# Optimization experiments

Hardware: AMD Instinct MI355X
Metric: run time of the kernel (lower is better)

Reference implementation:

```python
import jax, jax.numpy as jnp
import numpy as np

B, T, C = 2, 4096, 768
H = 12
HD = C // H  # 64


def setup_inputs() -> dict:
    key = jax.random.key(0)
    k1, k2, k3 = jax.random.split(key, 3)
    scale = 0.02
    x = jax.random.normal(k1, (B, T, C), dtype=jnp.float32)
    w_attn = jax.random.normal(k2, (C, 3 * C), dtype=jnp.float32) * scale
    b_attn = jnp.zeros((3 * C,), dtype=jnp.float32)
    w_proj = jax.random.normal(k3, (C, C), dtype=jnp.float32) * scale
    b_proj = jnp.zeros((C,), dtype=jnp.float32)
    return {"x": x, "w_attn": w_attn, "b_attn": b_attn,
            "w_proj": w_proj, "b_proj": b_proj}


def reference(x, w_attn, b_attn, w_proj, b_proj):
    b, t, c = x.shape
    # QKV projection: (B,T,3C)
    qkv = x @ w_attn + b_attn
    q, k, v = jnp.split(qkv, 3, axis=2)
    # (B,H,T,HD)
    q = q.reshape(b, t, H, HD).transpose(0, 2, 1, 3)
    k = k.reshape(b, t, H, HD).transpose(0, 2, 1, 3)
    v = v.reshape(b, t, H, HD).transpose(0, 2, 1, 3)
    # scores: (B,H,T,T)
    scores = jnp.einsum('bhqd,bhkd->bhqk', q, k) / jnp.sqrt(jnp.float32(HD))
    causal = jnp.tril(jnp.ones((t, t), dtype=bool))
    scores = jnp.where(causal[None, None, :, :], scores, -jnp.inf)
    att = jax.nn.softmax(scores, axis=-1)
    # attn_dropout p=0 -> identity
    y = jnp.einsum('bhqk,bhkd->bhqd', att, v)
    y = y.transpose(0, 2, 1, 3).reshape(b, t, c)
    # output projection (resid_dropout p=0 -> identity)
    return y @ w_proj + b_proj
```

## Files before the change

kernel.cpp:

```cpp
#include <hip/hip_runtime.h>


typedef unsigned short u16;
typedef unsigned int u32;
using bf16x8 = __attribute__((ext_vector_type(8))) short;
using f32x4  = __attribute__((ext_vector_type(4))) float;

__device__ __forceinline__ float bf2f(u16 u) {
  return __uint_as_float(((u32)u) << 16);
}
__device__ __forceinline__ u16 f2bf(float f) {
  u32 u = __float_as_uint(f);
  u += 0x7fffu + ((u >> 16) & 1u);
  return (u16)(u >> 16);
}
__device__ __forceinline__ u32 cvtpk(float lo, float hi) {
  u32 r;
  asm("v_cvt_pk_bf16_f32 %0, %1, %2" : "=v"(r) : "v"(lo), "v"(hi));
  return r;
}
__device__ __forceinline__ void gload_lds16(const u16* g, u16* l) {
  __builtin_amdgcn_global_load_lds(
      (const __attribute__((address_space(1))) unsigned int*)g,
      (__attribute__((address_space(3))) unsigned int*)l, 16, 0, 0);
}

__global__ void fill_sentinel_f32(float* __restrict__ out, int n, float v) {
  const int i0 = blockIdx.x * blockDim.x + threadIdx.x;
  const int stride = gridDim.x * blockDim.x;
  for (int i = i0; i < n; i += stride) out[i] = v;
}

__global__ __launch_bounds__(256)
void prep(const float* __restrict__ x, const float* __restrict__ w_attn,
          const float* __restrict__ b_attn, const float* __restrict__ w_proj,
          const float* __restrict__ b_proj, u16* __restrict__ xb,
          u16* __restrict__ WtA, u16* __restrict__ WtP,
          u16* __restrict__ ba, u16* __restrict__ bp) {
  __shared__ u16 tile[32][33];
  const int bid = blockIdx.x, tid = threadIdx.x;
  if (bid < 2304) {
    const float* in; u16* out; int R, C, bx, by;
    if (bid < 1728) { in = w_attn; out = WtA; R = 768; C = 2304;
                      bx = bid % 72; by = bid / 72; }
    else            { in = w_proj; out = WtP; R = 768; C = 768;
                      bx = (bid - 1728) % 24; by = (bid - 1728) / 24; }
    const int c0 = bx * 32, r0 = by * 32;
    const int tx = tid & 31, ty = tid >> 5;
#pragma unroll
    for (int i = 0; i < 32; i += 8)
      tile[ty + i][tx] = f2bf(in[(size_t)(r0 + ty + i) * C + c0 + tx]);
    __syncthreads();
#pragma unroll
    for (int i = 0; i < 32; i += 8)
      out[(size_t)(c0 + ty + i) * R + r0 + tx] = tile[tx][ty + i];
  } else if (bid < 3328) {
    const int n4 = 8192 * 768 / 4;
    const int i0 = (bid - 2304) * 256 + tid, stride = 1024 * 256;
    const float4* src = (const float4*)x;
    ushort4* dst = (ushort4*)xb;
    for (int i = i0; i < n4; i += stride) {
      const float4 v = src[i];
      ushort4 o;
      o.x = f2bf(v.x); o.y = f2bf(v.y); o.z = f2bf(v.z); o.w = f2bf(v.w);
      dst[i] = o;
    }
  } else {
    for (int i = tid; i < 2304; i += 256) ba[i] = f2bf(b_attn[i]);
    for (int i = tid; i < 768; i += 256) bp[i] = f2bf(b_proj[i]);
  }
}

#define QSCALE 0.18033688011112f

__global__ __launch_bounds__(256, 3)
void gemm128(const u16* __restrict__ A, const u16* __restrict__ Bt,
             const u16* __restrict__ bias, u16* __restrict__ O0,
             u16* __restrict__ O1, u16* __restrict__ O2, int Kd) {
  __shared__ __align__(16) u16 As[128 * 64];
  __shared__ __align__(16) u16 Bs[128 * 64];
  const int tid = threadIdx.x;
  const int lane = tid & 63, wave = tid >> 6;
  const int wm = wave >> 1, wn = wave & 1;
  const int l16 = lane & 15, quad = lane >> 4;

  const u16* Ag0 = A + (size_t)blockIdx.x * 128 * Kd +
                   (size_t)(tid >> 3) * Kd + (tid & 7) * 8;
  const u16* Bg0 = Bt + (size_t)blockIdx.y * 128 * Kd +
                   (size_t)(tid >> 3) * Kd + (tid & 7) * 8;
  const int ldsb = wave * 512;

  f32x4 acc[4][4] = {};
  for (int kt = 0; kt < Kd; kt += 64) {
#pragma unroll
    for (int i = 0; i < 4; ++i) {
      gload_lds16(Ag0 + (size_t)i * 32 * Kd + kt, &As[i * 2048 + ldsb]);
      gload_lds16(Bg0 + (size_t)i * 32 * Kd + kt, &Bs[i * 2048 + ldsb]);
    }
    __syncthreads();
#pragma unroll
    for (int s = 0; s < 2; ++s) {
      bf16x8 af[4], bfr[4];
#pragma unroll
      for (int i = 0; i < 4; ++i) {
        const int m = wm * 64 + i * 16 + l16;
        af[i] = *(const bf16x8*)&As[m * 64 + (s * 4 + quad) * 8];
        const int n = wn * 64 + i * 16 + l16;
        bfr[i] = *(const bf16x8*)&Bs[n * 64 + (s * 4 + quad) * 8];
      }
#pragma unroll
      for (int i = 0; i < 4; ++i)
#pragma unroll
        for (int j = 0; j < 4; ++j)
          acc[i][j] = __builtin_amdgcn_mfma_f32_16x16x32_bf16(af[i], bfr[j],
                                                              acc[i][j], 0, 0, 0);
    }
    __syncthreads();
  }

#pragma unroll
  for (int i = 0; i < 4; ++i) {
    const int mbase = blockIdx.x * 128 + wm * 64 + i * 16 + quad * 4;
#pragma unroll
    for (int j = 0; j < 4; ++j) {
      const int nb = blockIdx.y * 128 + wn * 64 + j * 16;
      const int n = nb + l16;
      const float bv = bf2f(bias[n]);
      const int which = nb / 768;
      const int b = mbase >> 12, t = mbase & 4095;
      const int c = n - which * 768;
      const int h = c >> 6, d = c & 63;
      const size_t bh = (size_t)b * 12 + h;
      if (which == 0) {
#pragma unroll
        for (int r = 0; r < 4; ++r)
          O0[((bh * 4096 + t + r) << 6) + d] =
              f2bf((acc[i][j][r] + bv) * QSCALE);
      } else if (which == 1) {
#pragma unroll
        for (int r = 0; r < 4; ++r)
          O1[((bh * 4096 + t + r) << 6) + d] = f2bf(acc[i][j][r] + bv);
      } else {
        ushort4 pk;
        pk.x = f2bf(acc[i][j][0] + bv);
        pk.y = f2bf(acc[i][j][1] + bv);
        pk.z = f2bf(acc[i][j][2] + bv);
        pk.w = f2bf(acc[i][j][3] + bv);
        *(ushort4*)&O2[((bh << 6) + (size_t)d) * 4096 + t] = pk;
      }
    }
  }
}

__global__ __launch_bounds__(256, 3)
void gemm_n64(const u16* __restrict__ A, const u16* __restrict__ Bt,
              const u16* __restrict__ bias, float* __restrict__ out, int Kd) {
  __shared__ __align__(16) u16 As[128 * 64];
  __shared__ __align__(16) u16 Bs[64 * 64];
  const int tid = threadIdx.x;
  const int lane = tid & 63, wave = tid >> 6;
  const int l16 = lane & 15, quad = lane >> 4;

  const u16* Ag0 = A + (size_t)blockIdx.x * 128 * Kd +
                   (size_t)(tid >> 3) * Kd + (tid & 7) * 8;
  const u16* Bg0 = Bt + (size_t)blockIdx.y * 64 * Kd +
                   (size_t)(tid >> 3) * Kd + (tid & 7) * 8;
  const int ldsb = wave * 512;

  f32x4 acc[2][4] = {};
  for (int kt = 0; kt < Kd; kt += 64) {
#pragma unroll
    for (int i = 0; i < 4; ++i)
      gload_lds16(Ag0 + (size_t)i * 32 * Kd + kt, &As[i * 2048 + ldsb]);
#pragma unroll
    for (int i = 0; i < 2; ++i)
      gload_lds16(Bg0 + (size_t)i * 32 * Kd + kt, &Bs[i * 2048 + ldsb]);
    __syncthreads();
#pragma unroll
    for (int s = 0; s < 2; ++s) {
      bf16x8 af[2], bfr[4];
#pragma unroll
      for (int i = 0; i < 2; ++i) {
        const int m = wave * 32 + i * 16 + l16;
        af[i] = *(const bf16x8*)&As[m * 64 + (s * 4 + quad) * 8];
      }
#pragma unroll
      for (int j = 0; j < 4; ++j) {
        const int n = j * 16 + l16;
        bfr[j] = *(const bf16x8*)&Bs[n * 64 + (s * 4 + quad) * 8];
      }
#pragma unroll
      for (int i = 0; i < 2; ++i)
#pragma unroll
        for (int j = 0; j < 4; ++j)
          acc[i][j] = __builtin_amdgcn_mfma_f32_16x16x32_bf16(af[i], bfr[j],
                                                              acc[i][j], 0, 0, 0);
    }
    __syncthreads();
  }

#pragma unroll
  for (int i = 0; i < 2; ++i) {
    const int mbase = blockIdx.x * 128 + wave * 32 + i * 16 + quad * 4;
#pragma unroll
    for (int j = 0; j < 4; ++j) {
      const int n = blockIdx.y * 64 + j * 16 + l16;
      const float bv = bf2f(bias[n]);
#pragma unroll
      for (int r = 0; r < 4; ++r)
        out[(size_t)(mbase + r) * 768 + n] = acc[i][j][r] + bv;
    }
  }
}

__global__ __launch_bounds__(256, 3)
void attn_chunk(const u16* __restrict__ Q, const u16* __restrict__ K,
                const u16* __restrict__ Vt, u16* __restrict__ Y,
                u16* __restrict__ part_o, float* __restrict__ part_l) {
  const int idx = blockIdx.x;
  const int bh = idx % 24;
  const int cid = 79 - (idx / 24);
  int qt = 0, base = 0, nc = 1;
  for (int q = 0; q < 32; ++q) {
    const int c = (q >> 3) + 1;
    if (cid < base + c) { qt = q; nc = c; break; }
    base += c;
  }
  const int j = cid - base;
  const int Nt = 2 * qt + 2;
  const int kbeg = j * 16;
  const int kend = (kbeg + 16 < Nt) ? kbeg + 16 : Nt;
  const int q0 = qt * 128;
  const int b = bh / 12, h = bh % 12;
  const size_t ho = (size_t)bh * 4096 * 64;
  const u16* Qg = Q + ho + (size_t)q0 * 64;
  const u16* Kg = K + ho;
  const u16* Vg = Vt + ho;

  __shared__ __align__(16) u16 Ks[3][64 * 64];
  __shared__ __align__(16) u16 Vs[3][64 * 64];

  const int tid = threadIdx.x;
  const int lane = tid & 63, wave = tid >> 6;
  const int l16 = lane & 15, quad = lane >> 4;
  const int sw8 = (l16 & 7) * 8;

  const int rl = tid >> 3, m7 = tid & 7;
  const int cs = (m7 ^ (rl & 7)) * 8;
  const u16* kg0 = Kg + (size_t)rl * 64 + cs;
  const u16* vg0 = Vg + (size_t)rl * 4096 + cs;
  const int wb = wave * 512;

  bf16x8 qf[2][2];
#pragma unroll
  for (int rt = 0; rt < 2; ++rt)
#pragma unroll
    for (int s = 0; s < 2; ++s)
      qf[rt][s] = *(const bf16x8*)&Qg[(wave * 32 + rt * 16 + l16) * 64 + s * 32 + quad * 8];

  bf16x8 ones;
#pragma unroll
  for (int e = 0; e < 8; ++e) ones[e] = (short)0x3F80;

  f32x4 lacc[2] = {};
  f32x4 o[2][4] = {};

  auto stage = [&](int bf, int kt2) {
    const size_t ko = (size_t)kt2 * 4096;
    const int to = kt2 * 64;
    gload_lds16(kg0 + ko,               &Ks[bf][wb]);
    gload_lds16(kg0 + ko + 2048,        &Ks[bf][2048 + wb]);
    gload_lds16(vg0 + to,               &Vs[bf][wb]);
    gload_lds16(vg0 + to + 32 * 4096,   &Vs[bf][2048 + wb]);
  };

  const int ntt = kend - kbeg;
  stage(0, kbeg);
  if (ntt > 1) {
    stage(1, kbeg + 1);
    asm volatile("s_waitcnt vmcnt(4)" ::: "memory");
  } else {
    asm volatile("s_waitcnt vmcnt(0)" ::: "memory");
  }
  __builtin_amdgcn_sched_barrier(0);
  __builtin_amdgcn_s_barrier();
  int cur = 0;

  for (int kt2 = kbeg; kt2 < kend; ++kt2) {
    const int t0 = kt2 * 64;
    const bool pf = (kt2 + 2 < kend);
    if (pf) {
      int nb = cur + 2; if (nb >= 3) nb -= 3;
      stage(nb, kt2 + 2);
    }
    __builtin_amdgcn_sched_barrier(0);

    f32x4 sc[4][2] = {};
#pragma unroll
    for (int s = 0; s < 2; ++s) {
      bf16x8 kf[4];
#pragma unroll
      for (int nt = 0; nt < 4; ++nt)
        kf[nt] = *(const bf16x8*)&Ks[cur][(nt * 16 + l16) * 64 +
                                          ((s * 32 + quad * 8) ^ sw8)];
      __builtin_amdgcn_s_setprio(1);
#pragma unroll
      for (int nt = 0; nt < 4; ++nt)
#pragma unroll
        for (int rt = 0; rt < 2; ++rt)
          sc[nt][rt] = __builtin_amdgcn_mfma_f32_16x16x32_bf16(kf[nt], qf[rt][s],
                                                               sc[nt][rt], 0, 0, 0);
      __builtin_amdgcn_s_setprio(0);
    }

    u32 pw[4][2][2];
#pragma unroll
    for (int rt = 0; rt < 2; ++rt) {
      const int rowb = q0 + wave * 32 + rt * 16;
      if (t0 + 63 <= rowb) {
#pragma unroll
        for (int nt = 0; nt < 4; ++nt) {
          f32x4 p;
#pragma unroll
          for (int r = 0; r < 4; ++r)
            p[r] = __builtin_amdgcn_exp2f(sc[nt][rt][r]);
          pw[nt][rt][0] = cvtpk(p[0], p[1]);
          pw[nt][rt][1] = cvtpk(p[2], p[3]);
        }
      } else {
        const int qrow = rowb + l16;
#pragma unroll
        for (int nt = 0; nt < 4; ++nt) {
          f32x4 p;
#pragma unroll
          for (int r = 0; r < 4; ++r) {
            float pv = __builtin_amdgcn_exp2f(sc[nt][rt][r]);
            if (t0 + nt * 16 + quad * 4 + r > qrow) pv = 0.f;
            p[r] = pv;
          }
          pw[nt][rt][0] = cvtpk(p[0], p[1]);
          pw[nt][rt][1] = cvtpk(p[2], p[3]);
        }
      }
    }

#pragma unroll
    for (int s2 = 0; s2 < 2; ++s2) {
      bf16x8 vf[4];
#pragma unroll
      for (int dt = 0; dt < 4; ++dt) {
        const int vbase = (dt * 16 + l16) * 64;
        const int a1 = vbase + ((s2 * 32 + quad * 4) ^ sw8);
        union { uint2 hv[2]; bf16x8 v; } uv;
        uv.hv[0] = *(const uint2*)&Vs[cur][a1];
        uv.hv[1] = *(const uint2*)&Vs[cur][a1 ^ 16];
        vf[dt] = uv.v;
      }
#pragma unroll
      for (int rt = 0; rt < 2; ++rt) {
        union { u32 w[4]; bf16x8 v; } up;
        up.w[0] = pw[2 * s2][rt][0];
        up.w[1] = pw[2 * s2][rt][1];
        up.w[2] = pw[2 * s2 + 1][rt][0];
        up.w[3] = pw[2 * s2 + 1][rt][1];
        __builtin_amdgcn_s_setprio(1);
#pragma unroll
        for (int dt = 0; dt < 4; ++dt)
          o[rt][dt] = __builtin_amdgcn_mfma_f32_16x16x32_bf16(up.v, vf[dt],
                                                              o[rt][dt], 0, 0, 0);
        lacc[rt] = __builtin_amdgcn_mfma_f32_16x16x32_bf16(up.v, ones,
                                                           lacc[rt], 0, 0, 0);
        __builtin_amdgcn_s_setprio(0);
      }
    }

    if (kt2 + 1 < kend) {
      if (pf) asm volatile("s_waitcnt vmcnt(4)" ::: "memory");
      else    asm volatile("s_waitcnt vmcnt(0)" ::: "memory");
      __builtin_amdgcn_sched_barrier(0);
      __builtin_amdgcn_s_barrier();
      if (++cur == 3) cur = 0;
    }
  }

  if (nc == 1) {
#pragma unroll
    for (int rt = 0; rt < 2; ++rt)
#pragma unroll
      for (int r = 0; r < 4; ++r) {
        const float inv = 1.f / lacc[rt][r];
        const int t = q0 + wave * 32 + rt * 16 + quad * 4 + r;
#pragma unroll
        for (int dt = 0; dt < 4; ++dt)
          Y[((size_t)b * 4096 + t) * 768 + h * 64 + dt * 16 + l16] =
              f2bf(o[rt][dt][r] * inv);
      }
  } else {
    const int pslot = bh * 72 + (cid - 8);
    u16* po = part_o + (size_t)pslot * 8192;
    float* pl = part_l + pslot * 128;
#pragma unroll
    for (int rt = 0; rt < 2; ++rt)
#pragma unroll
      for (int r = 0; r < 4; ++r) {
        const int row = wave * 32 + rt * 16 + quad * 4 + r;
#pragma unroll
        for (int dt = 0; dt < 4; ++dt)
          po[row * 64 + dt * 16 + l16] = f2bf(o[rt][dt][r]);
        if (l16 == 0) pl[row] = lacc[rt][r];
      }
  }
}

__global__ __launch_bounds__(256, 8)
void attn_combine(const u16* __restrict__ part_o, const float* __restrict__ part_l,
                  u16* __restrict__ Y) {
  const int bh = blockIdx.x, qt = 8 + blockIdx.y;
  const int g = qt >> 3, i = qt & 7;
  const int nc = g + 1;
  const int base = 4 * g * (g + 1) + i * (g + 1);
  const int slot0 = bh * 72 + base - 8;
  const int b = bh / 12, h = bh % 12;
  const int q0 = qt * 128;
  for (int e = threadIdx.x; e < 8192; e += 256) {
    const int row = e >> 6, d = e & 63;
    float Os = 0.f, ls = 0.f;
    for (int c = 0; c < nc; ++c) {
      Os += bf2f(part_o[(size_t)(slot0 + c) * 8192 + e]);
      ls += part_l[(slot0 + c) * 128 + row];
    }
    Y[((size_t)b * 4096 + q0 + row) * 768 + h * 64 + d] = f2bf(Os / ls);
  }
}

extern "C" void kernel_launch(void* const* d_in, const int* in_sizes, int n_in,
                              void* d_out, int out_size, void* d_ws, size_t ws_size,
                              hipStream_t stream) {
  (void)in_sizes; (void)n_in;
  const float* x      = (const float*)d_in[0];
  const float* w_attn = (const float*)d_in[1];
  const float* b_attn = (const float*)d_in[2];
  const float* w_proj = (const float*)d_in[3];
  const float* b_proj = (const float*)d_in[4];
  float* out = (float*)d_out;

  char* ws = (char*)d_ws;
  size_t off = 0;
  auto alloc = [&](size_t bytes) -> void* {
    void* p = ws + off;
    off += (bytes + 255) & ~(size_t)255;
    return p;
  };
  u16* xb  = (u16*)alloc((size_t)8192 * 768 * 2);
  u16* WtA = (u16*)alloc((size_t)2304 * 768 * 2);
  u16* WtP = (u16*)alloc((size_t)768 * 768 * 2);
  u16* ba  = (u16*)alloc(2304 * 2);
  u16* bp  = (u16*)alloc(768 * 2);
  u16* Q   = (u16*)alloc((size_t)6291456 * 2);
  u16* Kp  = (u16*)alloc((size_t)6291456 * 2);
  u16* Vt  = (u16*)alloc((size_t)6291456 * 2);
  u16* Y   = (u16*)alloc((size_t)6291456 * 2);
  u16* part_o  = (u16*)alloc((size_t)24 * 72 * 8192 * 2);
  float* part_l = (float*)alloc((size_t)24 * 72 * 128 * 4);

  if (ws_size < off) {
    fill_sentinel_f32<<<256, 256, 0, stream>>>(out, out_size,
                                               100.0f + (float)(ws_size >> 20));
    return;
  }

  prep<<<3329, 256, 0, stream>>>(x, w_attn, b_attn, w_proj, b_proj,
                                 xb, WtA, WtP, ba, bp);
  gemm128<<<dim3(64, 18), 256, 0, stream>>>(xb, WtA, ba, Q, Kp, Vt, 768);
  attn_chunk<<<1920, 256, 0, stream>>>(Q, Kp, Vt, Y, part_o, part_l);
  attn_combine<<<dim3(24, 24), 256, 0, stream>>>(part_o, part_l, Y);
  gemm_n64<<<dim3(64, 12), 256, 0, stream>>>(Y, WtP, bp, out, 768);
}
```

Measured before the change: 266.9 us.

## Double-buffer GEMM LDS tiles and XOR-swizzle columns to avoid bank conflicts

Both projection GEMMs now use two LDS buffers and issue the global-to-LDS loads for the next K tile before computing on the current one, with one barrier per iteration instead of two. Source columns are XOR-swizzled by row when loading, and the fragment reads apply the matching swizzle to reduce LDS bank conflicts. gemm128 doubles its LDS use and drops its launch bound from 3 to 2 blocks per CU, which may lower occupancy. Only the GEMMs change; the attention kernel, which likely dominates runtime, is untouched.

```diff
diff --git a/kernel.cpp b/kernel.cpp
--- a/kernel.cpp
+++ b/kernel.cpp
@@ -73,40 +73,52 @@
 
 #define QSCALE 0.18033688011112f
 
-__global__ __launch_bounds__(256, 3)
+__global__ __launch_bounds__(256, 2)
 void gemm128(const u16* __restrict__ A, const u16* __restrict__ Bt,
              const u16* __restrict__ bias, u16* __restrict__ O0,
              u16* __restrict__ O1, u16* __restrict__ O2, int Kd) {
-  __shared__ __align__(16) u16 As[128 * 64];
-  __shared__ __align__(16) u16 Bs[128 * 64];
+  __shared__ __align__(16) u16 As[2][128 * 64];
+  __shared__ __align__(16) u16 Bs[2][128 * 64];
   const int tid = threadIdx.x;
   const int lane = tid & 63, wave = tid >> 6;
   const int wm = wave >> 1, wn = wave & 1;
   const int l16 = lane & 15, quad = lane >> 4;
-
-  const u16* Ag0 = A + (size_t)blockIdx.x * 128 * Kd +
-                   (size_t)(tid >> 3) * Kd + (tid & 7) * 8;
-  const u16* Bg0 = Bt + (size_t)blockIdx.y * 128 * Kd +
-                   (size_t)(tid >> 3) * Kd + (tid & 7) * 8;
+  const int swr = (l16 & 7) * 8;
+
+  const int rl = tid >> 3, m7 = tid & 7;
+  const int cs = (m7 ^ (rl & 7)) * 8;
+  const u16* Ag0 = A + (size_t)blockIdx.x * 128 * Kd + (size_t)rl * Kd + cs;
+  const u16* Bg0 = Bt + (size_t)blockIdx.y * 128 * Kd + (size_t)rl * Kd + cs;
   const int ldsb = wave * 512;
 
+  auto stage = [&](int bf, int kt) {
+#pragma unroll
+    for (int i = 0; i < 4; ++i) {
+      gload_lds16(Ag0 + (size_t)i * 32 * Kd + kt, &As[bf][i * 2048 + ldsb]);
+      gload_lds16(Bg0 + (size_t)i * 32 * Kd + kt, &Bs[bf][i * 2048 + ldsb]);
+    }
+  };
+
   f32x4 acc[4][4] = {};
+  stage(0, 0);
+  asm volatile("s_waitcnt vmcnt(0)" ::: "memory");
+  __builtin_amdgcn_sched_barrier(0);
+  __builtin_amdgcn_s_barrier();
+  int cur = 0;
+
   for (int kt = 0; kt < Kd; kt += 64) {
-#pragma unroll
-    for (int i = 0; i < 4; ++i) {
-      gload_lds16(Ag0 + (size_t)i * 32 * Kd + kt, &As[i * 2048 + ldsb]);
-      gload_lds16(Bg0 + (size_t)i * 32 * Kd + kt, &Bs[i * 2048 + ldsb]);
-    }
-    __syncthreads();
+    const bool more = (kt + 64 < Kd);
+    if (more) stage(cur ^ 1, kt + 64);
+    __builtin_amdgcn_sched_barrier(0);
 #pragma unroll
     for (int s = 0; s < 2; ++s) {
       bf16x8 af[4], bfr[4];
 #pragma unroll
       for (int i = 0; i < 4; ++i) {
         const int m = wm * 64 + i * 16 + l16;
-        af[i] = *(const bf16x8*)&As[m * 64 + (s * 4 + quad) * 8];
+        af[i] = *(const bf16x8*)&As[cur][m * 64 + (((s * 4 + quad) * 8) ^ swr)];
         const int n = wn * 64 + i * 16 + l16;
-        bfr[i] = *(const bf16x8*)&Bs[n * 64 + (s * 4 + quad) * 8];
+        bfr[i] = *(const bf16x8*)&Bs[cur][n * 64 + (((s * 4 + quad) * 8) ^ swr)];
       }
 #pragma unroll
       for (int i = 0; i < 4; ++i)
@@ -115,7 +127,12 @@
           acc[i][j] = __builtin_amdgcn_mfma_f32_16x16x32_bf16(af[i], bfr[j],
                                                               acc[i][j], 0, 0, 0);
     }
-    __syncthreads();
+    if (more) {
+      asm volatile("s_waitcnt vmcnt(0)" ::: "memory");
+      __builtin_amdgcn_sched_barrier(0);
+      __builtin_amdgcn_s_barrier();
+      cur ^= 1;
+    }
   }
 
 #pragma unroll
@@ -155,39 +172,51 @@
 __global__ __launch_bounds__(256, 3)
 void gemm_n64(const u16* __restrict__ A, const u16* __restrict__ Bt,
               const u16* __restrict__ bias, float* __restrict__ out, int Kd) {
-  __shared__ __align__(16) u16 As[128 * 64];
-  __shared__ __align__(16) u16 Bs[64 * 64];
+  __shared__ __align__(16) u16 As[2][128 * 64];
+  __shared__ __align__(16) u16 Bs[2][64 * 64];
   const int tid = threadIdx.x;
   const int lane = tid & 63, wave = tid >> 6;
   const int l16 = lane & 15, quad = lane >> 4;
-
-  const u16* Ag0 = A + (size_t)blockIdx.x * 128 * Kd +
-                   (size_t)(tid >> 3) * Kd + (tid & 7) * 8;
-  const u16* Bg0 = Bt + (size_t)blockIdx.y * 64 * Kd +
-                   (size_t)(tid >> 3) * Kd + (tid & 7) * 8;
+  const int swr = (l16 & 7) * 8;
+
+  const int rl = tid >> 3, m7 = tid & 7;
+  const int cs = (m7 ^ (rl & 7)) * 8;
+  const u16* Ag0 = A + (size_t)blockIdx.x * 128 * Kd + (size_t)rl * Kd + cs;
+  const u16* Bg0 = Bt + (size_t)blockIdx.y * 64 * Kd + (size_t)rl * Kd + cs;
   const int ldsb = wave * 512;
 
+  auto stage = [&](int bf, int kt) {
+#pragma unroll
+    for (int i = 0; i < 4; ++i)
+      gload_lds16(Ag0 + (size_t)i * 32 * Kd + kt, &As[bf][i * 2048 + ldsb]);
+#pragma unroll
+    for (int i = 0; i < 2; ++i)
+      gload_lds16(Bg0 + (size_t)i * 32 * Kd + kt, &Bs[bf][i * 2048 + ldsb]);
+  };
+
   f32x4 acc[2][4] = {};
+  stage(0, 0);
+  asm volatile("s_waitcnt vmcnt(0)" ::: "memory");
+  __builtin_amdgcn_sched_barrier(0);
+  __builtin_amdgcn_s_barrier();
+  int cur = 0;
+
   for (int kt = 0; kt < Kd; kt += 64) {
-#pragma unroll
-    for (int i = 0; i < 4; ++i)
-      gload_lds16(Ag0 + (size_t)i * 32 * Kd + kt, &As[i * 2048 + ldsb]);
-#pragma unroll
-    for (int i = 0; i < 2; ++i)
-      gload_lds16(Bg0 + (size_t)i * 32 * Kd + kt, &Bs[i * 2048 + ldsb]);
-    __syncthreads();
+    const bool more = (kt + 64 < Kd);
+    if (more) stage(cur ^ 1, kt + 64);
+    __builtin_amdgcn_sched_barrier(0);
 #pragma unroll
     for (int s = 0; s < 2; ++s) {
       bf16x8 af[2], bfr[4];
 #pragma unroll
       for (int i = 0; i < 2; ++i) {
         const int m = wave * 32 + i * 16 + l16;
-        af[i] = *(const bf16x8*)&As[m * 64 + (s * 4 + quad) * 8];
+        af[i] = *(const bf16x8*)&As[cur][m * 64 + (((s * 4 + quad) * 8) ^ swr)];
       }
 #pragma unroll
       for (int j = 0; j < 4; ++j) {
         const int n = j * 16 + l16;
-        bfr[j] = *(const bf16x8*)&Bs[n * 64 + (s * 4 + quad) * 8];
+        bfr[j] = *(const bf16x8*)&Bs[cur][n * 64 + (((s * 4 + quad) * 8) ^ swr)];
       }
 #pragma unroll
       for (int i = 0; i < 2; ++i)
@@ -196,7 +225,12 @@
           acc[i][j] = __builtin_amdgcn_mfma_f32_16x16x32_bf16(af[i], bfr[j],
                                                               acc[i][j], 0, 0, 0);
     }
-    __syncthreads();
+    if (more) {
+      asm volatile("s_waitcnt vmcnt(0)" ::: "memory");
+      __builtin_amdgcn_sched_barrier(0);
+      __builtin_amdgcn_s_barrier();
+      cur ^= 1;
+    }
   }
 
 #pragma unroll
```

Measured after the change: 268.5 us. Within noise of the previous version (+0.6%).
